# Performance work log

Measured on AMD Instinct MI355X. Metric: run time of the kernel, lower is better.

## Reference

```python
import jax, jax.numpy as jnp
import numpy as np

N_NODES = 50000
N_EDGES = 50000  # per-node attention scores are used as per-hyperedge weights => M == N
IN_CH = 128
OUT_CH = 128
NNZ = 800000


def setup_inputs() -> dict:
    key = jax.random.key(0)
    k = jax.random.split(key, 7)
    x = jax.random.normal(k[0], (N_NODES, IN_CH), dtype=jnp.float32)
    node_idx = jax.random.randint(k[1], (NNZ,), 0, N_NODES)
    edge_idx = jax.random.randint(k[2], (NNZ,), 0, N_EDGES)
    hyperedge_index = jnp.stack([node_idx, edge_idx]).astype(jnp.int64)
    s_in = 1.0 / np.sqrt(IN_CH)
    attn_w = jax.random.uniform(k[3], (1, IN_CH), minval=-s_in, maxval=s_in, dtype=jnp.float32)
    attn_b = jax.random.uniform(k[4], (1,), minval=-s_in, maxval=s_in, dtype=jnp.float32)
    lin_w = jax.random.uniform(k[5], (OUT_CH, IN_CH), minval=-s_in, maxval=s_in, dtype=jnp.float32)
    bias = jax.random.uniform(k[6], (OUT_CH,), minval=-s_in, maxval=s_in, dtype=jnp.float32)
    return {"x": x, "hyperedge_index": hyperedge_index,
            "attn_w": attn_w, "attn_b": attn_b, "lin_w": lin_w, "bias": bias}


def reference(x, hyperedge_index, attn_w, attn_b, lin_w, bias):
    # x: [N, C_in]; hyperedge_index: [2, nnz] (row 0: node ids, row 1: hyperedge ids)
    node_idx = hyperedge_index[0]
    edge_idx = hyperedge_index[1]
    N = x.shape[0]
    M = N_EDGES

    # edge_weight = sigmoid(attn(x)) -> used as hyperedge_weight (per-edge, M == N)
    w = jax.nn.sigmoid(x @ attn_w.T + attn_b)[:, 0]            # [M]

    xl = x @ lin_w.T                                           # [N, C_out]

    # D_v = sum of incident hyperedge weights per node; D^{-1} with inf -> 0
    D = jax.ops.segment_sum(w[edge_idx], node_idx, num_segments=N)
    Dinv = jnp.where(D > 0, 1.0 / D, 0.0)                      # [N]

    # B_e = hyperedge degree; B^{-1} with inf -> 0
    ones = jnp.ones(edge_idx.shape, dtype=x.dtype)
    Bdeg = jax.ops.segment_sum(ones, edge_idx, num_segments=M)
    Binv = jnp.where(Bdeg > 0, 1.0 / Bdeg, 0.0)                # [M]

    # node -> hyperedge: message = B_e^{-1} * x_j, aggregated at edge e
    msg = Binv[edge_idx][:, None] * xl[node_idx]               # [nnz, C_out]
    e_feat = jax.ops.segment_sum(msg, edge_idx, num_segments=M)

    # hyperedge -> node: message = D_v^{-1} * e_feat, aggregated at node v
    out = jax.ops.segment_sum(e_feat[edge_idx], node_idx, num_segments=N)
    out = Dinv[:, None] * out

    return out + bias
```

## Files before the change

kernel.cpp:

```cpp
#include <hip/hip_runtime.h>
#include <math.h>

#define CH 128
#define CAP 64
#define RSB 9
#define RS  (1 << RSB)
#define CAPB 10240
#define PB 2048
#define NCHUNK 4
#define CSUB 4
#define IDS 128

typedef __attribute__((ext_vector_type(8))) short bf16x8;
typedef __attribute__((ext_vector_type(4))) float f32x4;

__device__ __forceinline__ unsigned short f2bf(float f) {
    union { float f; unsigned u; } v; v.f = f;
    unsigned r = v.u + 0x7FFF + ((v.u >> 16) & 1);
    return (unsigned short)(r >> 16);
}
__device__ __forceinline__ float bflo(unsigned u) {
    union { unsigned u; float f; } v; v.u = u << 16; return v.f;
}
__device__ __forceinline__ float bfhi(unsigned u) {
    union { unsigned u; float f; } v; v.u = u & 0xFFFF0000u; return v.f;
}
__device__ __forceinline__ unsigned pack2bf(float a, float b) {
    return (unsigned)f2bf(a) | ((unsigned)f2bf(b) << 16);
}

__global__ __launch_bounds__(256) void fused_main(const float* __restrict__ x,
                                                  const float* __restrict__ attn_w,
                                                  const float* __restrict__ attn_b,
                                                  const float* __restrict__ lw,
                                                  unsigned short* __restrict__ xl,
                                                  float* __restrict__ w,
                                                  int nStrips,
                                                  const int* __restrict__ nidx,
                                                  const int* __restrict__ eidx,
                                                  int* __restrict__ binCnt,
                                                  unsigned int* __restrict__ binData,
                                                  int nnz, int nbd, int SB) {
    __shared__ unsigned short wl[128 * 136];
    __shared__ float awl[128];
    if ((int)blockIdx.x < SB) {
        int* hist = (int*)wl;
        int* base = ((int*)wl) + 256;
        int nbt = 2 * nbd;
        for (int i = threadIdx.x; i < nbt; i += 256) hist[i] = 0;
        __syncthreads();
        int k0 = blockIdx.x * PB + threadIdx.x;
        int vv[8], ee[8], sE[8], sN[8];
#pragma unroll
        for (int u = 0; u < 8; ++u) {
            int k = k0 + u * 256;
            if (k < nnz) {
                int v = nidx[k], e = eidx[k];
                vv[u] = v; ee[u] = e;
                sE[u] = atomicAdd(&hist[e >> RSB], 1);
                sN[u] = atomicAdd(&hist[nbd + (v >> RSB)], 1);
            } else vv[u] = -1;
        }
        __syncthreads();
        for (int i = threadIdx.x; i < nbt; i += 256)
            if (hist[i]) base[i] = atomicAdd(&binCnt[i], hist[i]);
        __syncthreads();
#pragma unroll
        for (int u = 0; u < 8; ++u) {
            if (vv[u] < 0) continue;
            int bE = ee[u] >> RSB;
            int bN = nbd + (vv[u] >> RSB);
            int iE = min(base[bE] + sE[u], CAPB - 1);
            int iN = min(base[bN] + sN[u], CAPB - 1);
            binData[(size_t)bE * CAPB + iE] = ((unsigned)ee[u] << 16) | (unsigned)vv[u];
            binData[(size_t)bN * CAPB + iN] = ((unsigned)vv[u] << 16) | (unsigned)ee[u];
        }
        return;
    }
    int tid = threadIdx.x;
    for (int i = tid; i < 2048; i += 256) {
        float4 vlo = ((const float4*)lw)[2 * i];
        float4 vhi = ((const float4*)lw)[2 * i + 1];
        int4 dst;
        dst.x = (int)pack2bf(vlo.x, vlo.y);
        dst.y = (int)pack2bf(vlo.z, vlo.w);
        dst.z = (int)pack2bf(vhi.x, vhi.y);
        dst.w = (int)pack2bf(vhi.z, vhi.w);
        *(int4*)(wl + (i >> 4) * 136 + (i & 15) * 8) = dst;
    }
    if (tid < 128) awl[tid] = attn_w[tid];
    float ab = attn_b[0];
    __syncthreads();
    int gb = blockIdx.x - SB;
    int wid = (gb << 2) | (tid >> 6);
    int lane = tid & 63;
    int m = lane & 15, quad = lane >> 4;
    int nWaves = ((int)gridDim.x - SB) << 2;
    size_t cs = (size_t)nStrips * 16 * 32;
    for (int s = wid; s < nStrips; s += nWaves) {
        int r0 = s << 4;
        const float* xr = x + (size_t)(r0 + m) * CH + quad * 8;
        float att = 0.f;
        bf16x8 a0, a1, a2, a3;
#define LOAD_FRAG(AFRAG, F)                                                   \
        {                                                                     \
            float4 lo = *(const float4*)(xr + (F) * 32);                      \
            float4 hi = *(const float4*)(xr + (F) * 32 + 4);                  \
            const float* ap = &awl[(F) * 32 + quad * 8];                      \
            att += lo.x * ap[0] + lo.y * ap[1] + lo.z * ap[2] + lo.w * ap[3]  \
                 + hi.x * ap[4] + hi.y * ap[5] + hi.z * ap[6] + hi.w * ap[7]; \
            union { int4 i; bf16x8 v; } pk;                                   \
            pk.i.x = (int)pack2bf(lo.x, lo.y);                                \
            pk.i.y = (int)pack2bf(lo.z, lo.w);                                \
            pk.i.z = (int)pack2bf(hi.x, hi.y);                                \
            pk.i.w = (int)pack2bf(hi.z, hi.w);                                \
            AFRAG = pk.v;                                                     \
        }
        LOAD_FRAG(a0, 0)
        LOAD_FRAG(a1, 1)
        LOAD_FRAG(a2, 2)
        LOAD_FRAG(a3, 3)
#undef LOAD_FRAG
        att += __shfl_xor(att, 16, 64);
        att += __shfl_xor(att, 32, 64);
        if (quad == 0) w[r0 + m] = 1.0f / (1.0f + expf(-(att + ab)));
        unsigned short* ob = xl + (size_t)(r0 + m) * 32 + quad * 4;
#pragma unroll
        for (int c0 = 0; c0 < 128; c0 += 16) {
            const unsigned short* wr = wl + (c0 + m) * 136 + quad * 8;
            f32x4 acc = {0.f, 0.f, 0.f, 0.f};
            acc = __builtin_amdgcn_mfma_f32_16x16x32_bf16(*(const bf16x8*)(wr),      a0, acc, 0, 0, 0);
            acc = __builtin_amdgcn_mfma_f32_16x16x32_bf16(*(const bf16x8*)(wr + 32), a1, acc, 0, 0, 0);
            acc = __builtin_amdgcn_mfma_f32_16x16x32_bf16(*(const bf16x8*)(wr + 64), a2, acc, 0, 0, 0);
            acc = __builtin_amdgcn_mfma_f32_16x16x32_bf16(*(const bf16x8*)(wr + 96), a3, acc, 0, 0, 0);
            uint2 o;
            o.x = pack2bf(acc[0], acc[1]);
            o.y = pack2bf(acc[2], acc[3]);
            *(uint2*)(ob + (size_t)(c0 >> 5) * cs + (c0 & 16)) = o;
        }
    }
}

__global__ __launch_bounds__(512, 8) void edge_agg(const int* __restrict__ binCnt,
                                                   const unsigned int* __restrict__ binData,
                                                   const unsigned short* __restrict__ xl,
                                                   unsigned short* __restrict__ ef,
                                                   int M, int rows) {
    __shared__ unsigned short bucket[IDS * CAP];
    __shared__ int cl[IDS];
    int bid = blockIdx.x;
    int chunk = bid & (NCHUNK - 1);
    int t = bid >> 2;
    int cb = t >> 2;
    int sr = t & (CSUB - 1);
    int idBase = (cb << RSB) + (sr << 7);
    for (int i = threadIdx.x; i < IDS; i += 512) cl[i] = 0;
    __syncthreads();
    int n = min(binCnt[cb], CAPB);
    const unsigned int* src = binData + (size_t)cb * CAPB;
#define SCAN1(E) { int lid = (int)((E) >> 16) - idBase;                        \
                   if ((unsigned)lid < IDS) {                                  \
                       int r = atomicAdd(&cl[lid], 1);                         \
                       bucket[(lid << 6) + min(r, CAP - 1)] =                  \
                           (unsigned short)((E) & 0xFFFFu); } }
    for (int i0 = (int)threadIdx.x << 2; i0 < n; i0 += 2048) {
        if (i0 + 4 <= n) {
            uint4 e4 = *(const uint4*)(src + i0);
            SCAN1(e4.x) SCAN1(e4.y) SCAN1(e4.z) SCAN1(e4.w)
        } else {
            for (int i = i0; i < n; ++i) { unsigned int e1 = src[i]; SCAN1(e1) }
        }
    }
    __syncthreads();
    size_t cbase = (size_t)chunk * rows * 32;
    int wid = threadIdx.x >> 6, lane = threadIdx.x & 63;
    int g = lane >> 3, gl = lane & 7;
    const unsigned short* bse = xl + cbase + (gl << 2);
    for (int li = wid; li < IDS; li += 8) {
        int gid = idBase + li;
        if (gid >= M) break;
        int deg = cl[li];
        int dl = min(deg, CAP);
        const unsigned short* col = bucket + (li << 6);
        float4 acc = {0.f, 0.f, 0.f, 0.f};
        int j = 0;
#define ROW2(M0, M1) { uint2 u0 = *(const uint2*)(bse + (size_t)(M0) * 32);     \
                       uint2 u1 = *(const uint2*)(bse + (size_t)(M1) * 32);     \
                       acc.x += bflo(u0.x) + bflo(u1.x);                        \
                       acc.y += bfhi(u0.x) + bfhi(u1.x);                        \
                       acc.z += bflo(u0.y) + bflo(u1.y);                        \
                       acc.w += bfhi(u0.y) + bfhi(u1.y); }
#define ROW1(M0)     { uint2 u0 = *(const uint2*)(bse + (size_t)(M0) * 32);     \
                       acc.x += bflo(u0.x); acc.y += bfhi(u0.x);                \
                       acc.z += bflo(u0.y); acc.w += bfhi(u0.y); }
        for (; j + 16 <= dl; j += 16) { int m0 = col[j + g], m1 = col[j + 8 + g]; ROW2(m0, m1) }
        if (j + 8 <= dl) { int m0 = col[j + g]; ROW1(m0) j += 8; }
        { int rem = dl - j; if (g < rem) { int m0 = col[j + g]; ROW1(m0) } }
#undef ROW2
#undef ROW1
        acc.x += __shfl_xor(acc.x, 8, 64);  acc.y += __shfl_xor(acc.y, 8, 64);
        acc.z += __shfl_xor(acc.z, 8, 64);  acc.w += __shfl_xor(acc.w, 8, 64);
        acc.x += __shfl_xor(acc.x, 16, 64); acc.y += __shfl_xor(acc.y, 16, 64);
        acc.z += __shfl_xor(acc.z, 16, 64); acc.w += __shfl_xor(acc.w, 16, 64);
        acc.x += __shfl_xor(acc.x, 32, 64); acc.y += __shfl_xor(acc.y, 32, 64);
        acc.z += __shfl_xor(acc.z, 32, 64); acc.w += __shfl_xor(acc.w, 32, 64);
        if (g == 0) {
            float binv = deg > 0 ? 1.0f / (float)deg : 0.0f;
            uint2 o;
            o.x = pack2bf(acc.x * binv, acc.y * binv);
            o.y = pack2bf(acc.z * binv, acc.w * binv);
            *(uint2*)(ef + cbase + (size_t)gid * 32 + (gl << 2)) = o;
        }
    }
}

__global__ __launch_bounds__(512, 8) void node_agg(const int* __restrict__ binCnt,
                                                   const unsigned int* __restrict__ binData,
                                                   const unsigned short* __restrict__ ef,
                                                   const float* __restrict__ w,
                                                   const float* __restrict__ bias,
                                                   float* __restrict__ out,
                                                   int N, int rows) {
    __shared__ unsigned short bucket[IDS * CAP];
    __shared__ int cl[IDS];
    int bid = blockIdx.x;
    int chunk = bid & (NCHUNK - 1);
    int t = bid >> 2;
    int cb = t >> 2;
    int sr = t & (CSUB - 1);
    int idBase = (cb << RSB) + (sr << 7);
    for (int i = threadIdx.x; i < IDS; i += 512) cl[i] = 0;
    __syncthreads();
    int n = min(binCnt[cb], CAPB);
    const unsigned int* src = binData + (size_t)cb * CAPB;
    for (int i0 = (int)threadIdx.x << 2; i0 < n; i0 += 2048) {
        if (i0 + 4 <= n) {
            uint4 e4 = *(const uint4*)(src + i0);
            SCAN1(e4.x) SCAN1(e4.y) SCAN1(e4.z) SCAN1(e4.w)
        } else {
            for (int i = i0; i < n; ++i) { unsigned int e1 = src[i]; SCAN1(e1) }
        }
    }
#undef SCAN1
    __syncthreads();
    size_t cbase = (size_t)chunk * rows * 32;
    int wid = threadIdx.x >> 6, lane = threadIdx.x & 63;
    int g = lane >> 3, gl = lane & 7;
    const unsigned short* bse = ef + cbase + (gl << 2);
    for (int li = wid; li < IDS; li += 8) {
        int gid = idBase + li;
        if (gid >= N) break;
        int deg = cl[li];
        int dl = min(deg, CAP);
        const unsigned short* col = bucket + (li << 6);
        float4 acc = {0.f, 0.f, 0.f, 0.f};
        float ds = 0.f;
        int j = 0;
#define ROW2(M0, M1) { uint2 u0 = *(const uint2*)(bse + (size_t)(M0) * 32);     \
                       uint2 u1 = *(const uint2*)(bse + (size_t)(M1) * 32);     \
                       ds += w[M0] + w[M1];                                     \
                       acc.x += bflo(u0.x) + bflo(u1.x);                        \
                       acc.y += bfhi(u0.x) + bfhi(u1.x);                        \
                       acc.z += bflo(u0.y) + bflo(u1.y);                        \
                       acc.w += bfhi(u0.y) + bfhi(u1.y); }
#define ROW1(M0)     { uint2 u0 = *(const uint2*)(bse + (size_t)(M0) * 32);     \
                       ds += w[M0];                                             \
                       acc.x += bflo(u0.x); acc.y += bfhi(u0.x);                \
                       acc.z += bflo(u0.y); acc.w += bfhi(u0.y); }
        for (; j + 16 <= dl; j += 16) { int m0 = col[j + g], m1 = col[j + 8 + g]; ROW2(m0, m1) }
        if (j + 8 <= dl) { int m0 = col[j + g]; ROW1(m0) j += 8; }
        { int rem = dl - j; if (g < rem) { int m0 = col[j + g]; ROW1(m0) } }
#undef ROW2
#undef ROW1
        acc.x += __shfl_xor(acc.x, 8, 64);  acc.y += __shfl_xor(acc.y, 8, 64);
        acc.z += __shfl_xor(acc.z, 8, 64);  acc.w += __shfl_xor(acc.w, 8, 64);
        ds    += __shfl_xor(ds, 8, 64);
        acc.x += __shfl_xor(acc.x, 16, 64); acc.y += __shfl_xor(acc.y, 16, 64);
        acc.z += __shfl_xor(acc.z, 16, 64); acc.w += __shfl_xor(acc.w, 16, 64);
        ds    += __shfl_xor(ds, 16, 64);
        acc.x += __shfl_xor(acc.x, 32, 64); acc.y += __shfl_xor(acc.y, 32, 64);
        acc.z += __shfl_xor(acc.z, 32, 64); acc.w += __shfl_xor(acc.w, 32, 64);
        ds    += __shfl_xor(ds, 32, 64);
        if (g == 0) {
            float dinv = ds > 0.f ? 1.0f / ds : 0.0f;
            float4 bi = *(const float4*)(bias + chunk * 32 + (gl << 2));
            float4 o;
            o.x = acc.x * dinv + bi.x;
            o.y = acc.y * dinv + bi.y;
            o.z = acc.z * dinv + bi.z;
            o.w = acc.w * dinv + bi.w;
            *(float4*)(out + (size_t)gid * CH + chunk * 32 + (gl << 2)) = o;
        }
    }
}

extern "C" void kernel_launch(void* const* d_in, const int* in_sizes, int n_in,
                              void* d_out, int out_size, void* d_ws, size_t ws_size,
                              hipStream_t stream) {
    const float* x      = (const float*)d_in[0];
    const int*   hei    = (const int*)d_in[1];
    const float* attn_w = (const float*)d_in[2];
    const float* attn_b = (const float*)d_in[3];
    const float* lin_w  = (const float*)d_in[4];
    const float* bias   = (const float*)d_in[5];
    float* out = (float*)d_out;

    const int N   = in_sizes[0] / CH;
    const int nnz = in_sizes[1] / 2;
    const int* nidx = hei;
    const int* eidx = hei + nnz;

    unsigned short* efbf = (unsigned short*)d_ws;
    float*          w    = (float*)(efbf + (size_t)N * CH);
    unsigned int*   binData = (unsigned int*)(w + N);
    int nbd = (N + RS - 1) >> RSB;
    int*            binCnt  = (int*)(binData + (size_t)2 * nbd * CAPB);

    unsigned short* xlbf = (unsigned short*)out;

    hipMemsetAsync(binCnt, 0, (size_t)2 * nbd * sizeof(int), stream);

    int SB = (nnz + PB - 1) / PB;
    int nStrips = N / 16;
    int GB = (nStrips + 3) / 4;
    fused_main<<<SB + GB, 256, 0, stream>>>(x, attn_w, attn_b, lin_w, xlbf, w,
                                            nStrips, nidx, eidx, binCnt, binData,
                                            nnz, nbd, SB);

    int aggGrid = nbd * CSUB * NCHUNK;
    edge_agg<<<aggGrid, 512, 0, stream>>>(binCnt, binData, xlbf, efbf, N, N);
    node_agg<<<aggGrid, 512, 0, stream>>>(binCnt + nbd,
                                          binData + (size_t)nbd * CAPB,
                                          efbf, w, bias, out, N, N);
}
```

Measured before the change: 217.0 us.

## Build per-id adjacency buckets once in separate kernel, reuse across channel chunks

Adds a bucket_build kernel that scans each bin once and writes fixed-capacity per-id column lists and counts to global memory, and also precomputes the inverse node degree. Previously every channel-chunk block rescanned its whole bin with shared-memory atomics, repeating the scan NCHUNK times per id range in both aggregation kernels. The aggregation kernels now just copy a precomputed bucket into LDS. The gather loops are unrolled to four rows per step. This adds an extra launch plus global writes and reads of the column arrays, and the dinv loop is serial per thread.

```diff
diff --git a/kernel.cpp b/kernel.cpp
--- a/kernel.cpp
+++ b/kernel.cpp
@@ -8,8 +8,8 @@
 #define CAPB 10240
 #define PB 2048
 #define NCHUNK 4
-#define CSUB 4
 #define IDS 128
+#define BPB 2
 
 typedef __attribute__((ext_vector_type(8))) short bf16x8;
 typedef __attribute__((ext_vector_type(4))) float f32x4;
@@ -141,8 +141,59 @@
     }
 }
 
-__global__ __launch_bounds__(512, 8) void edge_agg(const int* __restrict__ binCnt,
-                                                   const unsigned int* __restrict__ binData,
+__global__ __launch_bounds__(256) void bucket_build(const int* __restrict__ binCnt,
+                                                    const unsigned int* __restrict__ binData,
+                                                    const float* __restrict__ w,
+                                                    int* __restrict__ cntE,
+                                                    unsigned short* __restrict__ colE,
+                                                    int* __restrict__ cntN,
+                                                    unsigned short* __restrict__ colN,
+                                                    float* __restrict__ dinv,
+                                                    int nbd, int N) {
+    __shared__ int cl[256];
+    int b = blockIdx.x;
+    int isN = b >= nbd * BPB;
+    int t = isN ? b - nbd * BPB : b;
+    int bin = t >> 1, half = t & 1;
+    int idBase = (bin << RSB) + (half << 8);
+    int* cnt = isN ? cntN : cntE;
+    unsigned short* col = isN ? colN : colE;
+    cl[threadIdx.x] = 0;
+    __syncthreads();
+    int bi = bin + (isN ? nbd : 0);
+    int n = min(binCnt[bi], CAPB);
+    const unsigned int* src = binData + (size_t)bi * CAPB;
+#define SCAN1(E) { int lid = (int)((E) >> 16) - idBase;                        \
+                   if ((unsigned)lid < 256u) {                                 \
+                       int r = atomicAdd(&cl[lid], 1);                         \
+                       col[(size_t)(idBase + lid) * CAP + min(r, CAP - 1)] =   \
+                           (unsigned short)((E) & 0xFFFFu); } }
+    for (int i0 = (int)threadIdx.x << 2; i0 < n; i0 += 1024) {
+        if (i0 + 4 <= n) {
+            uint4 e4 = *(const uint4*)(src + i0);
+            SCAN1(e4.x) SCAN1(e4.y) SCAN1(e4.z) SCAN1(e4.w)
+        } else {
+            for (int i = i0; i < n; ++i) { unsigned int e1 = src[i]; SCAN1(e1) }
+        }
+    }
+#undef SCAN1
+    __syncthreads();
+    int gid = idBase + threadIdx.x;
+    if (gid < N) {
+        int c = cl[threadIdx.x];
+        cnt[gid] = c;
+        if (isN) {
+            int dl = min(c, CAP);
+            const unsigned short* cc = col + (size_t)gid * CAP;
+            float ds = 0.f;
+            for (int j = 0; j < dl; ++j) ds += w[cc[j]];
+            dinv[gid] = ds > 0.f ? 1.0f / ds : 0.0f;
+        }
+    }
+}
+
+__global__ __launch_bounds__(512, 8) void edge_agg(const int* __restrict__ cntE,
+                                                   const unsigned short* __restrict__ colE,
                                                    const unsigned short* __restrict__ xl,
                                                    unsigned short* __restrict__ ef,
                                                    int M, int rows) {
@@ -150,32 +201,35 @@
     __shared__ int cl[IDS];
     int bid = blockIdx.x;
     int chunk = bid & (NCHUNK - 1);
-    int t = bid >> 2;
-    int cb = t >> 2;
-    int sr = t & (CSUB - 1);
-    int idBase = (cb << RSB) + (sr << 7);
-    for (int i = threadIdx.x; i < IDS; i += 512) cl[i] = 0;
-    __syncthreads();
-    int n = min(binCnt[cb], CAPB);
-    const unsigned int* src = binData + (size_t)cb * CAPB;
-#define SCAN1(E) { int lid = (int)((E) >> 16) - idBase;                        \
-                   if ((unsigned)lid < IDS) {                                  \
-                       int r = atomicAdd(&cl[lid], 1);                         \
-                       bucket[(lid << 6) + min(r, CAP - 1)] =                  \
-                           (unsigned short)((E) & 0xFFFFu); } }
-    for (int i0 = (int)threadIdx.x << 2; i0 < n; i0 += 2048) {
-        if (i0 + 4 <= n) {
-            uint4 e4 = *(const uint4*)(src + i0);
-            SCAN1(e4.x) SCAN1(e4.y) SCAN1(e4.z) SCAN1(e4.w)
-        } else {
-            for (int i = i0; i < n; ++i) { unsigned int e1 = src[i]; SCAN1(e1) }
-        }
+    int ib = bid >> 2;
+    int idBase = ib << 7;
+    if (threadIdx.x < IDS) {
+        int gid = idBase + threadIdx.x;
+        cl[threadIdx.x] = (gid < M) ? cntE[gid] : 0;
+    }
+    {
+        const uint4* s = (const uint4*)(colE + (size_t)idBase * CAP);
+        uint4* d = (uint4*)bucket;
+        for (int i = threadIdx.x; i < IDS * CAP / 8; i += 512) d[i] = s[i];
     }
     __syncthreads();
     size_t cbase = (size_t)chunk * rows * 32;
     int wid = threadIdx.x >> 6, lane = threadIdx.x & 63;
     int g = lane >> 3, gl = lane & 7;
     const unsigned short* bse = xl + cbase + (gl << 2);
+#define ROW4(M0, M1, M2, M3) {                                                  \
+        uint2 u0 = *(const uint2*)(bse + (size_t)(M0) * 32);                    \
+        uint2 u1 = *(const uint2*)(bse + (size_t)(M1) * 32);                    \
+        uint2 u2 = *(const uint2*)(bse + (size_t)(M2) * 32);                    \
+        uint2 u3 = *(const uint2*)(bse + (size_t)(M3) * 32);                    \
+        acc.x += bflo(u0.x) + bflo(u1.x) + bflo(u2.x) + bflo(u3.x);             \
+        acc.y += bfhi(u0.x) + bfhi(u1.x) + bfhi(u2.x) + bfhi(u3.x);             \
+        acc.z += bflo(u0.y) + bflo(u1.y) + bflo(u2.y) + bflo(u3.y);             \
+        acc.w += bfhi(u0.y) + bfhi(u1.y) + bfhi(u2.y) + bfhi(u3.y); }
+#define ROW1(M0) {                                                              \
+        uint2 u0 = *(const uint2*)(bse + (size_t)(M0) * 32);                    \
+        acc.x += bflo(u0.x); acc.y += bfhi(u0.x);                               \
+        acc.z += bflo(u0.y); acc.w += bfhi(u0.y); }
     for (int li = wid; li < IDS; li += 8) {
         int gid = idBase + li;
         if (gid >= M) break;
@@ -184,20 +238,12 @@
         const unsigned short* col = bucket + (li << 6);
         float4 acc = {0.f, 0.f, 0.f, 0.f};
         int j = 0;
-#define ROW2(M0, M1) { uint2 u0 = *(const uint2*)(bse + (size_t)(M0) * 32);     \
-                       uint2 u1 = *(const uint2*)(bse + (size_t)(M1) * 32);     \
-                       acc.x += bflo(u0.x) + bflo(u1.x);                        \
-                       acc.y += bfhi(u0.x) + bfhi(u1.x);                        \
-                       acc.z += bflo(u0.y) + bflo(u1.y);                        \
-                       acc.w += bfhi(u0.y) + bfhi(u1.y); }
-#define ROW1(M0)     { uint2 u0 = *(const uint2*)(bse + (size_t)(M0) * 32);     \
-                       acc.x += bflo(u0.x); acc.y += bfhi(u0.x);                \
-                       acc.z += bflo(u0.y); acc.w += bfhi(u0.y); }
-        for (; j + 16 <= dl; j += 16) { int m0 = col[j + g], m1 = col[j + 8 + g]; ROW2(m0, m1) }
-        if (j + 8 <= dl) { int m0 = col[j + g]; ROW1(m0) j += 8; }
+        for (; j + 32 <= dl; j += 32) {
+            int m0 = col[j + g], m1 = col[j + 8 + g], m2 = col[j + 16 + g], m3 = col[j + 24 + g];
+            ROW4(m0, m1, m2, m3)
+        }
+        for (; j + 8 <= dl; j += 8) { int m0 = col[j + g]; ROW1(m0) }
         { int rem = dl - j; if (g < rem) { int m0 = col[j + g]; ROW1(m0) } }
-#undef ROW2
-#undef ROW1
         acc.x += __shfl_xor(acc.x, 8, 64);  acc.y += __shfl_xor(acc.y, 8, 64);
         acc.z += __shfl_xor(acc.z, 8, 64);  acc.w += __shfl_xor(acc.w, 8, 64);
         acc.x += __shfl_xor(acc.x, 16, 64); acc.y += __shfl_xor(acc.y, 16, 64);
@@ -212,12 +258,14 @@
             *(uint2*)(ef + cbase + (size_t)gid * 32 + (gl << 2)) = o;
         }
     }
-}
-
-__global__ __launch_bounds__(512, 8) void node_agg(const int* __restrict__ binCnt,
-                                                   const unsigned int* __restrict__ binData,
+#undef ROW4
+#undef ROW1
+}
+
+__global__ __launch_bounds__(512, 8) void node_agg(const int* __restrict__ cntN,
+                                                   const unsigned short* __restrict__ colN,
                                                    const unsigned short* __restrict__ ef,
-                                                   const float* __restrict__ w,
+                                                   const float* __restrict__ dinv,
                                                    const float* __restrict__ bias,
                                                    float* __restrict__ out,
                                                    int N, int rows) {
@@ -225,28 +273,35 @@
     __shared__ int cl[IDS];
     int bid = blockIdx.x;
     int chunk = bid & (NCHUNK - 1);
-    int t = bid >> 2;
-    int cb = t >> 2;
-    int sr = t & (CSUB - 1);
-    int idBase = (cb << RSB) + (sr << 7);
-    for (int i = threadIdx.x; i < IDS; i += 512) cl[i] = 0;
-    __syncthreads();
-    int n = min(binCnt[cb], CAPB);
-    const unsigned int* src = binData + (size_t)cb * CAPB;
-    for (int i0 = (int)threadIdx.x << 2; i0 < n; i0 += 2048) {
-        if (i0 + 4 <= n) {
-            uint4 e4 = *(const uint4*)(src + i0);
-            SCAN1(e4.x) SCAN1(e4.y) SCAN1(e4.z) SCAN1(e4.w)
-        } else {
-            for (int i = i0; i < n; ++i) { unsigned int e1 = src[i]; SCAN1(e1) }
-        }
-    }
-#undef SCAN1
+    int ib = bid >> 2;
+    int idBase = ib << 7;
+    if (threadIdx.x < IDS) {
+        int gid = idBase + threadIdx.x;
+        cl[threadIdx.x] = (gid < N) ? cntN[gid] : 0;
+    }
+    {
+        const uint4* s = (const uint4*)(colN + (size_t)idBase * CAP);
+        uint4* d = (uint4*)bucket;
+        for (int i = threadIdx.x; i < IDS * CAP / 8; i += 512) d[i] = s[i];
+    }
     __syncthreads();
     size_t cbase = (size_t)chunk * rows * 32;
     int wid = threadIdx.x >> 6, lane = threadIdx.x & 63;
     int g = lane >> 3, gl = lane & 7;
     const unsigned short* bse = ef + cbase + (gl << 2);
+#define ROW4(M0, M1, M2, M3) {                                                  \
+        uint2 u0 = *(const uint2*)(bse + (size_t)(M0) * 32);                    \
+        uint2 u1 = *(const uint2*)(bse + (size_t)(M1) * 32);                    \
+        uint2 u2 = *(const uint2*)(bse + (size_t)(M2) * 32);                    \
+        uint2 u3 = *(const uint2*)(bse + (size_t)(M3) * 32);                    \
+        acc.x += bflo(u0.x) + bflo(u1.x) + bflo(u2.x) + bflo(u3.x);             \
+        acc.y += bfhi(u0.x) + bfhi(u1.x) + bfhi(u2.x) + bfhi(u3.x);             \
+        acc.z += bflo(u0.y) + bflo(u1.y) + bflo(u2.y) + bflo(u3.y);             \
+        acc.w += bfhi(u0.y) + bfhi(u1.y) + bfhi(u2.y) + bfhi(u3.y); }
+#define ROW1(M0) {                                                              \
+        uint2 u0 = *(const uint2*)(bse + (size_t)(M0) * 32);                    \
+        acc.x += bflo(u0.x); acc.y += bfhi(u0.x);                               \
+        acc.z += bflo(u0.y); acc.w += bfhi(u0.y); }
     for (int li = wid; li < IDS; li += 8) {
         int gid = idBase + li;
         if (gid >= N) break;
@@ -254,44 +309,32 @@
         int dl = min(deg, CAP);
         const unsigned short* col = bucket + (li << 6);
         float4 acc = {0.f, 0.f, 0.f, 0.f};
-        float ds = 0.f;
         int j = 0;
-#define ROW2(M0, M1) { uint2 u0 = *(const uint2*)(bse + (size_t)(M0) * 32);     \
-                       uint2 u1 = *(const uint2*)(bse + (size_t)(M1) * 32);     \
-                       ds += w[M0] + w[M1];                                     \
-                       acc.x += bflo(u0.x) + bflo(u1.x);                        \
-                       acc.y += bfhi(u0.x) + bfhi(u1.x);                        \
-                       acc.z += bflo(u0.y) + bflo(u1.y);                        \
-                       acc.w += bfhi(u0.y) + bfhi(u1.y); }
-#define ROW1(M0)     { uint2 u0 = *(const uint2*)(bse + (size_t)(M0) * 32);     \
-                       ds += w[M0];                                             \
-                       acc.x += bflo(u0.x); acc.y += bfhi(u0.x);                \
-                       acc.z += bflo(u0.y); acc.w += bfhi(u0.y); }
-        for (; j + 16 <= dl; j += 16) { int m0 = col[j + g], m1 = col[j + 8 + g]; ROW2(m0, m1) }
-        if (j + 8 <= dl) { int m0 = col[j + g]; ROW1(m0) j += 8; }
+        for (; j + 32 <= dl; j += 32) {
+            int m0 = col[j + g], m1 = col[j + 8 + g], m2 = col[j + 16 + g], m3 = col[j + 24 + g];
+            ROW4(m0, m1, m2, m3)
+        }
+        for (; j + 8 <= dl; j += 8) { int m0 = col[j + g]; ROW1(m0) }
         { int rem = dl - j; if (g < rem) { int m0 = col[j + g]; ROW1(m0) } }
-#undef ROW2
-#undef ROW1
         acc.x += __shfl_xor(acc.x, 8, 64);  acc.y += __shfl_xor(acc.y, 8, 64);
         acc.z += __shfl_xor(acc.z, 8, 64);  acc.w += __shfl_xor(acc.w, 8, 64);
-        ds    += __shfl_xor(ds, 8, 64);
         acc.x += __shfl_xor(acc.x, 16, 64); acc.y += __shfl_xor(acc.y, 16, 64);
         acc.z += __shfl_xor(acc.z, 16, 64); acc.w += __shfl_xor(acc.w, 16, 64);
-        ds    += __shfl_xor(ds, 16, 64);
         acc.x += __shfl_xor(acc.x, 32, 64); acc.y += __shfl_xor(acc.y, 32, 64);
         acc.z += __shfl_xor(acc.z, 32, 64); acc.w += __shfl_xor(acc.w, 32, 64);
-        ds    += __shfl_xor(ds, 32, 64);
         if (g == 0) {
-            float dinv = ds > 0.f ? 1.0f / ds : 0.0f;
+            float dv = dinv[gid];
             float4 bi = *(const float4*)(bias + chunk * 32 + (gl << 2));
             float4 o;
-            o.x = acc.x * dinv + bi.x;
-            o.y = acc.y * dinv + bi.y;
-            o.z = acc.z * dinv + bi.z;
-            o.w = acc.w * dinv + bi.w;
+            o.x = acc.x * dv + bi.x;
+            o.y = acc.y * dv + bi.y;
+            o.z = acc.z * dv + bi.z;
+            o.w = acc.w * dv + bi.w;
             *(float4*)(out + (size_t)gid * CH + chunk * 32 + (gl << 2)) = o;
         }
     }
+#undef ROW4
+#undef ROW1
 }
 
 extern "C" void kernel_launch(void* const* d_in, const int* in_sizes, int n_in,
@@ -310,10 +353,18 @@
     const int* nidx = hei;
     const int* eidx = hei + nnz;
 
+    int nbd = (N + RS - 1) >> RSB;
+    int idBlocks = (N + IDS - 1) / IDS;
+    int NP = idBlocks * IDS;
+
     unsigned short* efbf = (unsigned short*)d_ws;
-    float*          w    = (float*)(efbf + (size_t)N * CH);
-    unsigned int*   binData = (unsigned int*)(w + N);
-    int nbd = (N + RS - 1) >> RSB;
+    float*          w    = (float*)(efbf + (size_t)NCHUNK * N * 32);
+    float*          dinv = w + N;
+    int*            cntE = (int*)(dinv + N);
+    int*            cntN = cntE + N;
+    unsigned short* colE = (unsigned short*)(cntN + N);
+    unsigned short* colN = colE + (size_t)NP * CAP;
+    unsigned int*   binData = (unsigned int*)(colN + (size_t)NP * CAP);
     int*            binCnt  = (int*)(binData + (size_t)2 * nbd * CAPB);
 
     unsigned short* xlbf = (unsigned short*)out;
@@ -327,9 +378,11 @@
                                             nStrips, nidx, eidx, binCnt, binData,
                                             nnz, nbd, SB);
 
-    int aggGrid = nbd * CSUB * NCHUNK;
-    edge_agg<<<aggGrid, 512, 0, stream>>>(binCnt, binData, xlbf, efbf, N, N);
-    node_agg<<<aggGrid, 512, 0, stream>>>(binCnt + nbd,
-                                          binData + (size_t)nbd * CAPB,
-                                          efbf, w, bias, out, N, N);
-}
+    bucket_build<<<2 * nbd * BPB, 256, 0, stream>>>(binCnt, binData, w,
+                                                    cntE, colE, cntN, colN,
+                                                    dinv, nbd, N);
+
+    int aggGrid = idBlocks * NCHUNK;
+    edge_agg<<<aggGrid, 512, 0, stream>>>(cntE, colE, xlbf, efbf, N, N);
+    node_agg<<<aggGrid, 512, 0, stream>>>(cntN, colN, efbf, dinv, bias, out, N, N);
+}
```

After: 229.6 us. +5.8%, slower.
